# Kernel optimization log

Hardware: AMD Instinct MI355X
Metric: run time of the kernel (lower is better)

## Reference

```python
import jax, jax.numpy as jnp
import numpy as np

MAX_LEN = 4096
D_MODEL = 768
POS_EMBED_DIM = 65
MLP_WIDTH = 64
NUM_LAYERS = 2
ORDER = 2
BATCH = 4
FAST_DECAY_PCT = 0.3
SLOW_DECAY_PCT = 1.5
TARGET = 0.01
SHIFT = 0.0


def make_z(l):
    # PosEmbeddings.z_init: (l, 1 + 2*bands)
    bands = (POS_EMBED_DIM - 1) // 2
    t = jnp.linspace(0.0, 1.0, MAX_LEN)[:l, None]
    t_rescaled = jnp.linspace(0.0, MAX_LEN - 1, MAX_LEN)[:l, None]
    w = 2 * jnp.pi * t_rescaled / l
    f = jnp.linspace(1e-4, bands - 1, bands)[None]
    zc = jnp.exp(-1j * f * w)
    return jnp.concatenate([t, zc.real, zc.imag], axis=-1).astype(jnp.float32)


def fftconv(seq, filt, bias):
    # seq: (b, l, d); filt: (l, d); bias: (d,)
    seq_len = seq.shape[-2]
    fft_size = 2 * seq_len
    filter_f = jnp.fft.rfft(filt, n=fft_size, axis=-2) / fft_size
    seq_f = jnp.fft.rfft(seq, n=fft_size, axis=-2)
    y = jnp.fft.irfft(seq_f * filter_f, n=fft_size, norm='forward', axis=-2)[..., :seq_len, :]
    return y + seq * bias


def setup_inputs() -> dict:
    key = jax.random.key(0)
    ks = jax.random.split(key, 8)
    s_mlp = 1.0 / np.sqrt(MLP_WIDTH)
    s_in = 1.0 / np.sqrt(POS_EMBED_DIM)
    s_d = 1.0 / np.sqrt(D_MODEL)
    s_p = 1.0 / np.sqrt((ORDER + 1) * D_MODEL)
    return {
        'u': jax.random.normal(ks[0], (BATCH, MAX_LEN, D_MODEL), jnp.float32),
        'z': make_z(MAX_LEN),
        'fin_W': jax.random.normal(ks[1], (POS_EMBED_DIM, MLP_WIDTH), jnp.float32) * s_in,
        'fin_b': jnp.zeros((MLP_WIDTH,), jnp.float32),
        'freq': jnp.full((MLP_WIDTH,), 1.0, jnp.float32),
        'mid_W': jax.random.normal(ks[2], (NUM_LAYERS, MLP_WIDTH, MLP_WIDTH), jnp.float32) * s_mlp,
        'mid_b': jnp.zeros((NUM_LAYERS, MLP_WIDTH), jnp.float32),
        'fout_W': jax.random.normal(ks[3], (MLP_WIDTH, (ORDER - 1) * D_MODEL), jnp.float32) * s_mlp,
        'proj_W': jax.random.normal(ks[4], (D_MODEL, (ORDER + 1) * D_MODEL), jnp.float32) * s_d,
        'proj_b': jnp.zeros(((ORDER + 1) * D_MODEL,), jnp.float32),
        'conv_W': jax.random.normal(ks[5], (3, (ORDER + 1) * D_MODEL), jnp.float32) * 0.3,
        'conv_b': jnp.zeros(((ORDER + 1) * D_MODEL,), jnp.float32),
        'filt_bias': jax.random.normal(ks[6], (ORDER - 1, D_MODEL), jnp.float32),
        'out_W': jax.random.normal(ks[7], ((ORDER + 1) * D_MODEL // (ORDER + 1) * (ORDER + 1), D_MODEL), jnp.float32)[: (ORDER + 1) * D_MODEL // (ORDER + 1) * 0 + (ORDER + 1) * D_MODEL // (ORDER + 1), :] * 0 + jax.random.normal(ks[7], (D_MODEL, D_MODEL), jnp.float32) * s_d,
        'out_b': jnp.zeros((D_MODEL,), jnp.float32),
    }


def reference(u, z, fin_W, fin_b, freq, mid_W, mid_b, fout_W, proj_W, proj_b, conv_W, conv_b, filt_bias, out_W, out_b):
    l = min(u.shape[-2], MAX_LEN)
    t = jnp.linspace(0.0, 1.0, MAX_LEN)[:l, None]  # (l, 1)

    # HyenaFilter: implicit filter MLP with sine activations
    k = jnp.sin(freq * (z @ fin_W + fin_b))
    for i in range(NUM_LAYERS):
        k = jnp.sin(freq * (k @ mid_W[i] + mid_b[i]))
    k = k @ fout_W  # (l, (order-1)*d)
    filters = k.reshape(l, ORDER - 1, D_MODEL).transpose(1, 0, 2)  # (o, l, d)

    # ExponentialModulation
    max_decay = jnp.log(TARGET) / FAST_DECAY_PCT
    min_decay = jnp.log(TARGET) / SLOW_DECAY_PCT
    deltas = jnp.linspace(min_decay, max_decay, D_MODEL)
    decay = jnp.exp(-t * jnp.abs(deltas))  # (l, d)
    filters = filters * (decay + SHIFT)

    # input projection + depthwise causal conv (kernel 3)
    up = u @ proj_W + proj_b  # (b, l, 3d)
    pad = jnp.pad(up, ((0, 0), (2, 0), (0, 0)))
    uc = conv_W[0] * pad[:, :l] + conv_W[1] * pad[:, 1:l + 1] + conv_W[2] * pad[:, 2:l + 2] + conv_b

    parts = jnp.split(uc, ORDER + 1, axis=-1)
    x, v = parts[:-1], parts[-1]
    for o in range(ORDER - 1):
        v = fftconv(v * x[o], filters[o], filt_bias[o])
    y = (v * x[-1]) @ out_W + out_b
    return y
```

## Files before the change

kernel.cpp:

```cpp
#include <hip/hip_runtime.h>
#include <math.h>

#define MAX_LEN 4096
#define D_MODEL 768
#define PE_DIM 65
#define MLP_W 64
#define NBATCH 4
#define D3 2304
#define ROWS (NBATCH*MAX_LEN)

typedef unsigned short u16;
typedef unsigned int u32;
typedef float f4 __attribute__((ext_vector_type(4)));
typedef __bf16 bf16x8 __attribute__((ext_vector_type(8)));
typedef float f32x4 __attribute__((ext_vector_type(4)));

__device__ inline u16 f2bf(float x) {
    u32 u = __float_as_uint(x);
    u += 0x7fffu + ((u >> 16) & 1u);
    return (u16)(u >> 16);
}
__device__ inline float bf2f(u16 v) { return __uint_as_float((u32)v << 16); }
__device__ inline u32 pk2(float a, float b) {
    return (u32)f2bf(a) | ((u32)f2bf(b) << 16);
}

#define GLDS16(gp, lp) __builtin_amdgcn_global_load_lds( \
    (const __attribute__((address_space(1))) u32*)(gp), \
    (__attribute__((address_space(3))) u32*)(lp), 16, 0, 0)

__launch_bounds__(256)
__global__ void filter_mlp_kernel(const float* __restrict__ z,
                                  const float* __restrict__ fin_W,
                                  const float* __restrict__ fin_b,
                                  const float* __restrict__ freq,
                                  const float* __restrict__ mid_W,
                                  const float* __restrict__ mid_b,
                                  float* __restrict__ k3out)
{
    __shared__ __align__(16) float W1[PE_DIM*MLP_W];
    __shared__ __align__(16) float Wm[2*MLP_W*MLP_W];
    __shared__ __align__(16) float zs[16*PE_DIM];
    __shared__ __align__(16) float kb[2][16*MLP_W];
    int tid = threadIdx.x;
    int t0 = blockIdx.x * 16;
    for (int i = tid; i < PE_DIM*MLP_W; i += 256) W1[i] = fin_W[i];
    for (int i = tid; i < 2*MLP_W*MLP_W; i += 256) Wm[i] = mid_W[i];
    for (int i = tid; i < 16*PE_DIM; i += 256) zs[i] = z[(size_t)t0*PE_DIM + i];
    __syncthreads();

    int j = tid & 63, tl = tid >> 6;
    float fj = freq[j];
    float a[4];

    {
        float fb = fin_b[j];
        #pragma unroll
        for (int tt = 0; tt < 4; ++tt) a[tt] = fb;
        for (int i = 0; i < PE_DIM; ++i) {
            float w = W1[i*MLP_W + j];
            #pragma unroll
            for (int tt = 0; tt < 4; ++tt)
                a[tt] += zs[(tl + 4*tt)*PE_DIM + i] * w;
        }
        #pragma unroll
        for (int tt = 0; tt < 4; ++tt)
            kb[0][(tl + 4*tt)*MLP_W + j] = sinf(fj*a[tt]);
    }
    __syncthreads();
    {
        float mb = mid_b[j];
        #pragma unroll
        for (int tt = 0; tt < 4; ++tt) a[tt] = mb;
        for (int i = 0; i < MLP_W; ++i) {
            float w = Wm[i*MLP_W + j];
            #pragma unroll
            for (int tt = 0; tt < 4; ++tt)
                a[tt] += kb[0][(tl + 4*tt)*MLP_W + i] * w;
        }
        #pragma unroll
        for (int tt = 0; tt < 4; ++tt)
            kb[1][(tl + 4*tt)*MLP_W + j] = sinf(fj*a[tt]);
    }
    __syncthreads();
    {
        float mb = mid_b[MLP_W + j];
        #pragma unroll
        for (int tt = 0; tt < 4; ++tt) a[tt] = mb;
        for (int i = 0; i < MLP_W; ++i) {
            float w = Wm[MLP_W*MLP_W + i*MLP_W + j];
            #pragma unroll
            for (int tt = 0; tt < 4; ++tt)
                a[tt] += kb[1][(tl + 4*tt)*MLP_W + i] * w;
        }
        #pragma unroll
        for (int tt = 0; tt < 4; ++tt)
            k3out[(size_t)(t0 + tl + 4*tt)*MLP_W + j] = sinf(fj*a[tt]);
    }
}

__launch_bounds__(256)
__global__ void filter_out_kernel(const float* __restrict__ k3,
                                  const float* __restrict__ fout_W,
                                  float* __restrict__ hTt)
{
    __shared__ __align__(16) float ks[64*64];
    __shared__ __align__(16) float fs[64*132];
    int tid = threadIdx.x;
    int d0 = blockIdx.x * 128;
    int t0 = blockIdx.y * 64;

    for (int q = tid; q < 1024; q += 256)
        *(f4*)&ks[q*4] = *(const f4*)&k3[(size_t)t0*MLP_W + q*4];
    for (int q = tid; q < 2048; q += 256) {
        int i = q >> 5, c = q & 31;
        *(f4*)&fs[i*132 + c*4] = *(const f4*)&fout_W[(size_t)i*D_MODEL + d0 + c*4];
    }
    __syncthreads();

    int c = tid & 31;
    int t_base = (tid >> 5)*8;
    f4 acc[8];
    #pragma unroll
    for (int tt = 0; tt < 8; ++tt) acc[tt] = (f4){0.f,0.f,0.f,0.f};

    for (int i = 0; i < MLP_W; ++i) {
        f4 fv = *(const f4*)&fs[i*132 + c*4];
        #pragma unroll
        for (int tt = 0; tt < 8; ++tt) {
            float kv = ks[(t_base + tt)*MLP_W + i];
            acc[tt][0] += kv * fv[0];
            acc[tt][1] += kv * fv[1];
            acc[tt][2] += kv * fv[2];
            acc[tt][3] += kv * fv[3];
        }
    }

    const float MIND = -3.0701134573253944f;
    const float MAXD = -15.350567286626972f;
    #pragma unroll
    for (int tt = 0; tt < 8; ++tt) {
        int t = t0 + t_base + tt;
        float ttf = (float)t * (1.0f/(float)(MAX_LEN-1));
        f4 o;
        #pragma unroll
        for (int dd = 0; dd < 4; ++dd) {
            int d = d0 + 4*c + dd;
            float delta = MIND + (MAXD-MIND)*((float)d*(1.0f/(float)(D_MODEL-1)));
            o[dd] = acc[tt][dd] * expf(-ttf*fabsf(delta));
        }
        *(f4*)&hTt[(size_t)t*D_MODEL + d0 + 4*c] = o;
    }
}

__global__ void cast_bf16_kernel(const float* __restrict__ src,
                                 u16* __restrict__ dst, int n)
{
    int i = (blockIdx.x*256 + threadIdx.x)*8;
    if (i + 7 >= n) {
        for (int j = i; j < n; ++j) dst[j] = f2bf(src[j]);
        return;
    }
    float4 a = *(const float4*)(src + i);
    float4 b = *(const float4*)(src + i + 4);
    uint4 o;
    o.x = pk2(a.x, a.y);
    o.y = pk2(a.z, a.w);
    o.z = pk2(b.x, b.y);
    o.w = pk2(b.z, b.w);
    *(uint4*)(dst + i) = o;
}

__global__ void transpose_cast_kernel(const float* __restrict__ src,
                                      u16* __restrict__ dst, int R, int C)
{
    __shared__ u16 tile[64][65];
    int c0 = blockIdx.x*64, r0 = blockIdx.y*64;
    int tid = threadIdx.x;
    #pragma unroll
    for (int p = 0; p < 16; ++p) {
        int idx = tid + 256*p;
        int rr = idx >> 6, cc = idx & 63;
        tile[rr][cc] = f2bf(src[(size_t)(r0+rr)*C + c0 + cc]);
    }
    __syncthreads();
    #pragma unroll
    for (int p = 0; p < 16; ++p) {
        int idx = tid + 256*p;
        int cr = idx >> 6, rc = idx & 63;
        dst[(size_t)(c0+cr)*R + r0 + rc] = tile[rc][cr];
    }
}

__launch_bounds__(256)
__global__ void gemm_mfma_kernel(const u16* __restrict__ A,
                                 const u16* __restrict__ Bt,
                                 const float* __restrict__ bias,
                                 float* __restrict__ C,
                                 int M, int N, int K)
{
    __shared__ __align__(16) u16 As[128*32];
    __shared__ __align__(16) u16 Bs[128*32];
    int tid = threadIdx.x;
    int lane = tid & 63, w = tid >> 6;
    int wm = (w >> 1)*64, wn = (w & 1)*64;
    int lrow = lane & 15, lch = lane >> 4;
    int m0 = blockIdx.y * 128, n0 = blockIdx.x * 128;

    int srow = lane >> 2;
    int scol = (lane & 3)*8;
    const u16* Ag = A  + (size_t)(m0 + w*32 + srow)*K + scol;
    const u16* Bg = Bt + (size_t)(n0 + w*32 + srow)*K + scol;
    u16* AsW = As + w*1024;
    u16* BsW = Bs + w*1024;

    f32x4 acc[4][4];
    #pragma unroll
    for (int i = 0; i < 4; ++i)
        #pragma unroll
        for (int j = 0; j < 4; ++j)
            acc[i][j] = (f32x4){0.f,0.f,0.f,0.f};

    for (int k0 = 0; k0 < K; k0 += 32) {
        GLDS16(Ag + k0,            AsW);
        GLDS16(Ag + 16*(size_t)K + k0, AsW + 512);
        GLDS16(Bg + k0,            BsW);
        GLDS16(Bg + 16*(size_t)K + k0, BsW + 512);
        __syncthreads();
        bf16x8 af[4], bfr[4];
        #pragma unroll
        for (int i = 0; i < 4; ++i) {
            af[i]  = *(const bf16x8*)&As[(wm + i*16 + lrow)*32 + lch*8];
            bfr[i] = *(const bf16x8*)&Bs[(wn + i*16 + lrow)*32 + lch*8];
        }
        #pragma unroll
        for (int mt = 0; mt < 4; ++mt)
            #pragma unroll
            for (int nt = 0; nt < 4; ++nt)
                acc[mt][nt] = __builtin_amdgcn_mfma_f32_16x16x32_bf16(
                    af[mt], bfr[nt], acc[mt][nt], 0, 0, 0);
        __syncthreads();
    }
    #pragma unroll
    for (int nt = 0; nt < 4; ++nt) {
        int n = n0 + wn + nt*16 + lrow;
        float bv = bias[n];
        #pragma unroll
        for (int mt = 0; mt < 4; ++mt) {
            int m = m0 + wm + mt*16 + lch*4;
            #pragma unroll
            for (int r = 0; r < 4; ++r)
                C[(size_t)(m + r)*N + n] = acc[mt][nt][r] + bv;
        }
    }
}

__global__ void convprep_kernel(const float* __restrict__ up,
                                const float* __restrict__ conv_W,
                                const float* __restrict__ conv_b,
                                u16* __restrict__ seqbf,
                                float* __restrict__ gate)
{
    __shared__ float sb[64][65];
    int d0 = blockIdx.x * 64;
    int t0 = blockIdx.y * 64;
    int b  = blockIdx.z;
    int tid = threadIdx.x;
    #pragma unroll
    for (int i = 0; i < 16; ++i) {
        int idx = tid + 256*i;
        int trow = idx >> 6, dcol = idx & 63;
        int t = t0 + trow;
        int d = d0 + dcol;
        size_t r = ((size_t)b*MAX_LEN + t)*D3;
        float uc[3];
        #pragma unroll
        for (int g = 0; g < 3; ++g) {
            int c = d + g*D_MODEL;
            float u0 = up[r + c];
            float u1 = (t >= 1) ? up[r - D3 + c]   : 0.f;
            float u2 = (t >= 2) ? up[r - 2*D3 + c] : 0.f;
            uc[g] = conv_W[c]*u2 + conv_W[D3 + c]*u1 + conv_W[2*D3 + c]*u0 + conv_b[c];
        }
        sb[trow][dcol] = uc[0]*uc[2];
        gate[((size_t)b*MAX_LEN + t)*D_MODEL + d] = uc[1];
    }
    __syncthreads();
    #pragma unroll
    for (int i = 0; i < 16; ++i) {
        int idx = tid + 256*i;
        int drow = idx >> 6, tcol = idx & 63;
        seqbf[((size_t)b*D_MODEL + d0 + drow)*MAX_LEN + t0 + tcol] = f2bf(sb[tcol][drow]);
    }
}

__launch_bounds__(256)
__global__ void longconv_mfma_kernel(const u16* __restrict__ seqbf,
                                     const u16* __restrict__ hbf,
                                     const float* __restrict__ filt_bias,
                                     float* __restrict__ yT)
{
    __shared__ __align__(16) u16 sq[4*4896];
    __shared__ __align__(16) u16 hp[4112];
    __shared__ __align__(16) u16 A_s[16*648];

    int d   = blockIdx.x;
    int tid = threadIdx.x;
    int lane = tid & 63, w = tid >> 6;
    int lrow = lane & 15, lch = lane >> 4;

    for (int q = tid; q < 4*544; q += 256) {
        int b = q / 544, qq = q - b*544;
        int p = b*4896 + ((qq + (qq >> 3)) << 3);
        uint4 o = make_uint4(0u,0u,0u,0u);
        if (qq >= 32) o = *(const uint4*)&seqbf[((size_t)b*D_MODEL + d)*MAX_LEN + (size_t)(qq-32)*8];
        *(uint4*)&sq[p] = o;
    }
    for (int q = tid; q < 514; q += 256) {
        uint4 o = make_uint4(0u,0u,0u,0u);
        if (q >= 2) o = *(const uint4*)&hbf[(size_t)d*MAX_LEN + (size_t)(q-2)*8];
        *(uint4*)&hp[q*8] = o;
    }

    f32x4 acc[16];
    #pragma unroll
    for (int g = 0; g < 16; ++g) acc[g] = (f32x4){0.f,0.f,0.f,0.f};

    int slab_b = tid >> 4;
    int i_b    = tid & 15;
    u32* bld = (u32*)&A_s[slab_b*648 + i_b*40];

    const char* sqb = (const char*)(sq + w*4896);
    int Q0 = 30 + 2*lrow + lch;

#define MM(af_, bf_, gi) acc[gi] = __builtin_amdgcn_mfma_f32_16x16x32_bf16(af_, bf_, acc[gi], 0, 0, 0)
#define GB(gb, DO_CARRY)                                                      \
    {                                                                         \
        bf16x8 bc0, bc1, bc2, bc3;                                            \
        if (4*(gb)+0 >= gmin) bc0 = *(const bf16x8*)(bp + 576*(4*(gb)+0));    \
        if (4*(gb)+1 >= gmin) bc1 = *(const bf16x8*)(bp + 576*(4*(gb)+1));    \
        if (4*(gb)+2 >= gmin) bc2 = *(const bf16x8*)(bp + 576*(4*(gb)+2));    \
        if (4*(gb)+3 >= gmin) bc3 = *(const bf16x8*)(bp + 576*(4*(gb)+3));    \
        if (4*(gb)+0 >= gmin) MM(aA, bc0, 4*(gb)+0);                          \
        if (4*(gb)+1 >= gmin) MM(aA, bc1, 4*(gb)+1);                          \
        if (4*(gb)+2 >= gmin) MM(aA, bc2, 4*(gb)+2);                          \
        if (4*(gb)+3 >= gmin) MM(aA, bc3, 4*(gb)+3);                          \
        if ((DO_CARRY) && 4*(gb)-1 >= gmin) MM(aB, bcarry, 4*(gb));           \
        if (4*(gb)+0 >= gmin) MM(aB, bc0, 4*(gb)+1);                          \
        if (4*(gb)+1 >= gmin) MM(aB, bc1, 4*(gb)+2);                          \
        if (4*(gb)+2 >= gmin) MM(aB, bc2, 4*(gb)+3);                          \
        bcarry = bc3;                                                         \
    }

    #pragma unroll 1
    for (int p = 0; p < 8; ++p) {
        __syncthreads();
        {
            int hbase = 32 + 512*p + 32*slab_b + i_b;
            #pragma unroll
            for (int kk = 0; kk < 16; ++kk) {
                u16 v0 = hp[hbase - 2*kk];
                u16 v1 = hp[hbase - 2*kk - 1];
                bld[kk] = (u32)v0 | ((u32)v1 << 16);
            }
        }
        __syncthreads();
        int gmin = 2*p;
        for (int s = 0; s < 8; ++s) {
            bf16x8 aA = *(const bf16x8*)&A_s[ s   *648 + lrow*40 + lch*8];
            bf16x8 aB = *(const bf16x8*)&A_s[(s+8)*648 + lrow*40 + lch*8];
            int Qs = Q0 - 64*p - 4*s;
            const char* bp = sqb + (Qs*16 + (Qs >> 3)*16);
            bf16x8 bcarry;
            GB(0, 0)
            GB(1, 1)
            GB(2, 1)
            GB(3, 1)
        }
    }
#undef GB
#undef MM

    float fb = filt_bias[d];
    const u16* sqbu = sq + w*4896;
    float* dsty = yT + ((size_t)w*D_MODEL + d)*MAX_LEN;
    #pragma unroll
    for (int g = 0; g < 16; ++g) {
        int t0 = 256*g + 16*lrow + 4*lch;
        int elem = 256 + t0;
        int Q = elem >> 3;
        const u16* pv = &sqbu[(((Q + (Q >> 3)) << 3)) | (elem & 7)];
        ushort4 sv = *(const ushort4*)pv;
        f4 o;
        o[0] = acc[g][0] + fb*bf2f(sv.x);
        o[1] = acc[g][1] + fb*bf2f(sv.y);
        o[2] = acc[g][2] + fb*bf2f(sv.z);
        o[3] = acc[g][3] + fb*bf2f(sv.w);
        *(f4*)&dsty[t0] = o;
    }
}

__global__ void gatemul_kernel(const float* __restrict__ yT,
                               const float* __restrict__ gate,
                               u16* __restrict__ Afin)
{
    __shared__ float tb[64][65];
    int d0 = blockIdx.x * 64;
    int t0 = blockIdx.y * 64;
    int b  = blockIdx.z;
    int tid = threadIdx.x;
    #pragma unroll
    for (int i = 0; i < 16; ++i) {
        int idx = tid + 256*i;
        int drow = idx >> 6, tcol = idx & 63;
        tb[drow][tcol] = yT[((size_t)b*D_MODEL + d0 + drow)*MAX_LEN + t0 + tcol];
    }
    __syncthreads();
    #pragma unroll
    for (int i = 0; i < 16; ++i) {
        int idx = tid + 256*i;
        int trow = idx >> 6, dcol = idx & 63;
        size_t r = ((size_t)b*MAX_LEN + t0 + trow)*D_MODEL + d0 + dcol;
        Afin[r] = f2bf(tb[dcol][trow] * gate[r]);
    }
}

extern "C" void kernel_launch(void* const* d_in, const int* in_sizes, int n_in,
                              void* d_out, int out_size, void* d_ws, size_t ws_size,
                              hipStream_t stream)
{
    (void)in_sizes; (void)n_in; (void)out_size; (void)ws_size;
    const float* u      = (const float*)d_in[0];
    const float* z      = (const float*)d_in[1];
    const float* fin_W  = (const float*)d_in[2];
    const float* fin_b  = (const float*)d_in[3];
    const float* freq   = (const float*)d_in[4];
    const float* mid_W  = (const float*)d_in[5];
    const float* mid_b  = (const float*)d_in[6];
    const float* fout_W = (const float*)d_in[7];
    const float* proj_W = (const float*)d_in[8];
    const float* proj_b = (const float*)d_in[9];
    const float* conv_W = (const float*)d_in[10];
    const float* conv_b = (const float*)d_in[11];
    const float* fbias  = (const float*)d_in[12];
    const float* out_W  = (const float*)d_in[13];
    const float* out_b  = (const float*)d_in[14];
    float* out = (float*)d_out;

    float* ws    = (float*)d_ws;
    u16*   hbf   = (u16*)ws;
    float* up    = ws + 1572864;
    float* gate  = up + 37748736;
    u16*   seqbf = (u16*)(gate + 12582912);
    u16*   Abf   = (u16*)(gate + 12582912 + 6291456);
    u16*   BpT1  = (u16*)(gate + 12582912 + 2*6291456);
    u16*   BpT2  = (u16*)(gate + 12582912 + 2*6291456 + 884736);
    float* hTt   = up;
    float* yT    = up;
    u16*   Afinbf= (u16*)(up + 16777216);
    float* k3buf = gate;

    filter_mlp_kernel<<<MAX_LEN/16, 256, 0, stream>>>(z, fin_W, fin_b, freq,
                                                      mid_W, mid_b, k3buf);
    filter_out_kernel<<<dim3(D_MODEL/128, MAX_LEN/64), 256, 0, stream>>>(
        k3buf, fout_W, hTt);
    transpose_cast_kernel<<<dim3(D_MODEL/64, MAX_LEN/64), 256, 0, stream>>>(
        hTt, hbf, MAX_LEN, D_MODEL);
    cast_bf16_kernel<<<(ROWS*D_MODEL)/(256*8), 256, 0, stream>>>(u, Abf, ROWS*D_MODEL);
    transpose_cast_kernel<<<dim3(D3/64, D_MODEL/64), 256, 0, stream>>>(
        proj_W, BpT1, D_MODEL, D3);
    gemm_mfma_kernel<<<dim3(D3/128, ROWS/128), 256, 0, stream>>>(
        Abf, BpT1, proj_b, up, ROWS, D3, D_MODEL);
    convprep_kernel<<<dim3(D_MODEL/64, MAX_LEN/64, NBATCH), 256, 0, stream>>>(
        up, conv_W, conv_b, seqbf, gate);
    transpose_cast_kernel<<<dim3(D_MODEL/64, D_MODEL/64), 256, 0, stream>>>(
        out_W, BpT2, D_MODEL, D_MODEL);
    longconv_mfma_kernel<<<D_MODEL, 256, 0, stream>>>(seqbf, hbf, fbias, yT);
    gatemul_kernel<<<dim3(D_MODEL/64, MAX_LEN/64, NBATCH), 256, 0, stream>>>(
        yT, gate, Afinbf);
    gemm_mfma_kernel<<<dim3(D_MODEL/128, ROWS/128), 256, 0, stream>>>(
        Afinbf, BpT2, out_b, out, ROWS, D_MODEL, D_MODEL);
}
```

Before: 456.1 us.

## Restructure causal Toeplitz conv loop to keep filter A-tiles in registers

Reorders the outer loop so each pass stages a different slab of the filter Toeplitz matrix, then loads all 16 A fragments into registers once and reuses each loaded signal fragment across a triangular set of MFMAs. The goal is fewer LDS reads of signal fragments and no per-group predicate branching. The LDS staging loop also rotates its write order per slab, which looks aimed at reducing bank conflicts. In exchange, holding 16 A fragments plus 16 accumulators raises register pressure and may lower occupancy.

After: 401.7 us. 1.14x faster.

```diff
diff --git a/kernel.cpp b/kernel.cpp
--- a/kernel.cpp
+++ b/kernel.cpp
@@ -328,57 +328,42 @@
 
     int slab_b = tid >> 4;
     int i_b    = tid & 15;
+    int rot    = (slab_b & 3)*4;
     u32* bld = (u32*)&A_s[slab_b*648 + i_b*40];
 
     const char* sqb = (const char*)(sq + w*4896);
     int Q0 = 30 + 2*lrow + lch;
 
 #define MM(af_, bf_, gi) acc[gi] = __builtin_amdgcn_mfma_f32_16x16x32_bf16(af_, bf_, acc[gi], 0, 0, 0)
-#define GB(gb, DO_CARRY)                                                      \
-    {                                                                         \
-        bf16x8 bc0, bc1, bc2, bc3;                                            \
-        if (4*(gb)+0 >= gmin) bc0 = *(const bf16x8*)(bp + 576*(4*(gb)+0));    \
-        if (4*(gb)+1 >= gmin) bc1 = *(const bf16x8*)(bp + 576*(4*(gb)+1));    \
-        if (4*(gb)+2 >= gmin) bc2 = *(const bf16x8*)(bp + 576*(4*(gb)+2));    \
-        if (4*(gb)+3 >= gmin) bc3 = *(const bf16x8*)(bp + 576*(4*(gb)+3));    \
-        if (4*(gb)+0 >= gmin) MM(aA, bc0, 4*(gb)+0);                          \
-        if (4*(gb)+1 >= gmin) MM(aA, bc1, 4*(gb)+1);                          \
-        if (4*(gb)+2 >= gmin) MM(aA, bc2, 4*(gb)+2);                          \
-        if (4*(gb)+3 >= gmin) MM(aA, bc3, 4*(gb)+3);                          \
-        if ((DO_CARRY) && 4*(gb)-1 >= gmin) MM(aB, bcarry, 4*(gb));           \
-        if (4*(gb)+0 >= gmin) MM(aB, bc0, 4*(gb)+1);                          \
-        if (4*(gb)+1 >= gmin) MM(aB, bc1, 4*(gb)+2);                          \
-        if (4*(gb)+2 >= gmin) MM(aB, bc2, 4*(gb)+3);                          \
-        bcarry = bc3;                                                         \
-    }
 
     #pragma unroll 1
-    for (int p = 0; p < 8; ++p) {
+    for (int s = 0; s < 8; ++s) {
         __syncthreads();
         {
-            int hbase = 32 + 512*p + 32*slab_b + i_b;
-            #pragma unroll
-            for (int kk = 0; kk < 16; ++kk) {
+            int hbase = 32 + 256*slab_b + 32*s + i_b;
+            #pragma unroll
+            for (int j = 0; j < 16; ++j) {
+                int kk = (j + rot) & 15;
                 u16 v0 = hp[hbase - 2*kk];
                 u16 v1 = hp[hbase - 2*kk - 1];
                 bld[kk] = (u32)v0 | ((u32)v1 << 16);
             }
         }
         __syncthreads();
-        int gmin = 2*p;
-        for (int s = 0; s < 8; ++s) {
-            bf16x8 aA = *(const bf16x8*)&A_s[ s   *648 + lrow*40 + lch*8];
-            bf16x8 aB = *(const bf16x8*)&A_s[(s+8)*648 + lrow*40 + lch*8];
-            int Qs = Q0 - 64*p - 4*s;
-            const char* bp = sqb + (Qs*16 + (Qs >> 3)*16);
-            bf16x8 bcarry;
-            GB(0, 0)
-            GB(1, 1)
-            GB(2, 1)
-            GB(3, 1)
-        }
-    }
-#undef GB
+        bf16x8 aR[16];
+        #pragma unroll
+        for (int r = 0; r < 16; ++r)
+            aR[r] = *(const bf16x8*)&A_s[r*648 + lrow*40 + lch*8];
+        int Qs = Q0 - 4*s;
+        const char* bp = sqb + (Qs*16 + (Qs >> 3)*16);
+        #pragma unroll
+        for (int dlt = 0; dlt < 16; ++dlt) {
+            bf16x8 F = *(const bf16x8*)(bp + 576*dlt);
+            #pragma unroll
+            for (int r = 0; r < 16 - dlt; ++r)
+                MM(aR[r], F, r + dlt);
+        }
+    }
 #undef MM
 
     float fb = filt_bias[d];
```
